# Performance work log

Measured on AMD Instinct MI355X. Metric: run time of the kernel, lower is better.

## Reference

```python
import jax, jax.numpy as jnp
import numpy as np
from jax import lax


def ternarize(w):
    # TWN-style ternarization: threshold delta = 0.7*mean|w|, scale alpha =
    # mean |w| over surviving entries; straight-through in backward.
    aw = jnp.abs(w)
    delta = 0.7 * jnp.mean(aw)
    mask = (aw > delta).astype(w.dtype)
    alpha = jnp.sum(aw * mask) / jnp.maximum(jnp.sum(mask), 1.0)
    q = alpha * jnp.sign(w) * mask
    return w + lax.stop_gradient(q - w)


def conv2d(x, w, b):
    # x: [N,C,H,W], w: [O,I,kh,kw]
    y = lax.conv_general_dilated(x, w, window_strides=(1, 1), padding='VALID',
                                 dimension_numbers=('NCHW', 'OIHW', 'NCHW'))
    return y + b[None, :, None, None]


def maxpool2(x):
    return lax.reduce_window(x, -jnp.inf, lax.max,
                             window_dimensions=(1, 1, 2, 2),
                             window_strides=(1, 1, 2, 2), padding='VALID')


def setup_inputs() -> dict:
    key = jax.random.key(0)
    ks = jax.random.split(key, 11)
    n_classes = 10
    x = jax.random.normal(ks[0], (1024, 1, 32, 32), dtype=jnp.float32)
    # Kaiming-ish scaled params
    w1 = jax.random.normal(ks[1], (32, 1, 5, 5), jnp.float32) * (1.0 / np.sqrt(1 * 25))
    b1 = jnp.zeros((32,), jnp.float32)
    w2 = jax.random.normal(ks[2], (64, 32, 5, 5), jnp.float32) * (1.0 / np.sqrt(32 * 25))
    b2 = jnp.zeros((64,), jnp.float32)
    w3 = jax.random.normal(ks[3], (120, 64, 5, 5), jnp.float32) * (1.0 / np.sqrt(64 * 25))
    b3 = jnp.zeros((120,), jnp.float32)
    fw1 = jax.random.normal(ks[4], (84, 120), jnp.float32) * (1.0 / np.sqrt(120))
    fb1 = jnp.zeros((84,), jnp.float32)
    fw2 = jax.random.normal(ks[5], (n_classes, 84), jnp.float32) * (1.0 / np.sqrt(84))
    fb2 = jnp.zeros((n_classes,), jnp.float32)
    return {"x": x, "w1": w1, "b1": b1, "w2": w2, "b2": b2,
            "w3": w3, "b3": b3, "fw1": fw1, "fb1": fb1, "fw2": fw2, "fb2": fb2}


def reference(x, w1, b1, w2, b2, w3, b3, fw1, fb1, fw2, fb2):
    h = jnp.tanh(conv2d(x, ternarize(w1), b1))   # [N,32,28,28]
    h = maxpool2(h)                              # [N,32,14,14]
    h = jnp.tanh(conv2d(h, ternarize(w2), b2))   # [N,64,10,10]
    h = maxpool2(h)                              # [N,64,5,5]
    h = jnp.tanh(conv2d(h, ternarize(w3), b3))   # [N,120,1,1]
    h = h.reshape(h.shape[0], -1)                # [N,120]
    h = jnp.tanh(h @ ternarize(fw1).T + fb1)     # [N,84]
    logits = h @ ternarize(fw2).T + fb2          # [N,n_classes]
    probs = jax.nn.softmax(logits, axis=1)
    return (logits, probs)
```

## Files before the change

### kernel.cpp

```cpp
#include <hip/hip_runtime.h>
#include <hip/hip_bf16.h>
#include <math.h>


typedef __attribute__((ext_vector_type(8))) short bf16x8;
typedef __attribute__((ext_vector_type(4))) float f32x4;

static const size_t OFF_PB    = 0;
static const size_t OFF_W1B   = 256;
static const size_t OFF_W2B   = 1056;
static const size_t OFF_W3B   = 26656;
static const size_t OFF_FW1T  = 129056;
static const size_t OFF_FW2T  = 139136;
static const size_t OFF_P2B   = 139976;

#define BPT 16

__device__ __forceinline__ ushort f2bf(float v) {
    unsigned u = __float_as_uint(v);
    unsigned r = (u + 0x7FFFu + ((u >> 16) & 1u)) >> 16;
    return (ushort)r;
}
__device__ __forceinline__ float bf2f(ushort h) {
    return __uint_as_float((unsigned)h << 16);
}

__device__ __forceinline__ float tanh_fast(float x) {
    float e = __expf(-2.0f * fabsf(x));
    float r = 1.0f - 2.0f * e / (1.0f + e);
    return copysignf(r, x);
}

__device__ __forceinline__ void tensor_select(int tensor,
        const float* w1, const float* w2, const float* w3,
        const float* fw1, const float* fw2,
        const float*& src, int& O, int& K) {
    switch (tensor) {
        case 0: src = w1;  O = 32;  K = 25;   break;
        case 1: src = w2;  O = 64;  K = 800;  break;
        case 2: src = w3;  O = 120; K = 1600; break;
        case 3: src = fw1; O = 84;  K = 120;  break;
        default: src = fw2; O = 10; K = 84;   break;
    }
}

__device__ __forceinline__ float block_sum_256(float v, float* sbuf) {
    #pragma unroll
    for (int off = 32; off > 0; off >>= 1) v += __shfl_down(v, off);
    const int wid = threadIdx.x >> 6;
    if ((threadIdx.x & 63) == 0) sbuf[wid] = v;
    __syncthreads();
    return sbuf[0] + sbuf[1] + sbuf[2] + sbuf[3];
}

__device__ __forceinline__ float alpha_of(const float* pb, int tensor) {
    float s1 = 0.f, c = 0.f;
    #pragma unroll
    for (int i = 0; i < BPT; ++i) {
        s1 += pb[80 + tensor * BPT + i];
        c  += pb[160 + tensor * BPT + i];
    }
    return s1 / fmaxf(c, 1.0f);
}

__global__ __launch_bounds__(256)
void tern_pass1(const float* w1, const float* w2, const float* w3,
                const float* fw1, const float* fw2, float* pb) {
    __shared__ float sbuf[4];
    const int tensor = blockIdx.x / BPT;
    const int blk    = blockIdx.x % BPT;
    const float* src; int O, K;
    tensor_select(tensor, w1, w2, w3, fw1, fw2, src, O, K);
    const int n = O * K;
    float s = 0.f;
    for (int i = blk * 256 + threadIdx.x; i < n; i += BPT * 256)
        s += fabsf(src[i]);
    s = block_sum_256(s, sbuf);
    if (threadIdx.x == 0) pb[tensor * BPT + blk] = s;
}

__global__ __launch_bounds__(256)
void tern_pass2(const float* w1, const float* w2, const float* w3,
                const float* fw1, const float* fw2,
                ushort* w1b, ushort* w2b, ushort* w3b,
                float* fw1t, float* fw2t, float* pb) {
    __shared__ float sbuf[4];
    const int tensor = blockIdx.x / BPT;
    const int blk    = blockIdx.x % BPT;
    const float* src; int O, K;
    tensor_select(tensor, w1, w2, w3, fw1, fw2, src, O, K);
    const int n = O * K;
    float tot = 0.f;
    #pragma unroll
    for (int i = 0; i < BPT; ++i) tot += pb[tensor * BPT + i];
    const float delta = 0.7f * tot / (float)n;

    const ushort BP = 0x3F80u, BN = 0xBF80u;
    float s1 = 0.f, cnt = 0.f;

    if (tensor == 0) {
        for (int j = blk * 256 + threadIdx.x; j < 1024; j += BPT * 256) {
            const int oc = j >> 5, kk = j & 31;
            ushort qb = 0;
            if (kk < 25) {
                float w = src[oc * 25 + kk];
                float aw = fabsf(w);
                if (aw > delta) { s1 += aw; cnt += 1.f; qb = (w > 0.f) ? BP : BN; }
            }
            w1b[j] = qb;
        }
    } else if (tensor == 2) {
        for (int i = blk * 256 + threadIdx.x; i < 128 * 1600; i += BPT * 256) {
            ushort qb = 0;
            if (i < n) {
                float w = src[i];
                float aw = fabsf(w);
                if (aw > delta) { s1 += aw; cnt += 1.f; qb = (w > 0.f) ? BP : BN; }
            }
            w3b[i] = qb;
        }
    } else if (tensor == 1) {
        for (int i = blk * 256 + threadIdx.x; i < n; i += BPT * 256) {
            float w = src[i];
            float aw = fabsf(w);
            ushort qb = 0;
            if (aw > delta) { s1 += aw; cnt += 1.f; qb = (w > 0.f) ? BP : BN; }
            int oc = i / 800;
            int r  = i - oc * 800;
            int ic = r / 25;
            int tap = r - ic * 25;
            w2b[oc * 800 + tap * 32 + ic] = qb;
        }
    } else {
        float* dst = (tensor == 3) ? fw1t : fw2t;
        for (int i = blk * 256 + threadIdx.x; i < n; i += BPT * 256) {
            float w = src[i];
            float aw = fabsf(w);
            float q = 0.f;
            if (aw > delta) { s1 += aw; cnt += 1.f; q = (w > 0.f) ? 1.f : -1.f; }
            int o = i / K;
            int k = i - o * K;
            dst[k * O + o] = q;
        }
    }
    s1 = block_sum_256(s1, sbuf);
    __syncthreads();
    cnt = block_sum_256(cnt, sbuf);
    if (threadIdx.x == 0) {
        pb[80 + tensor * BPT + blk]  = s1;
        pb[160 + tensor * BPT + blk] = cnt;
    }
}

#define C2PF 4
__device__ __forceinline__ void conv2_all(
        const ushort* __restrict__ w2b, const ushort* sxt,
        int n0, int mt0, int lane, f32x4 acc[4][2]) {
    const int col = lane & 15, quad = lane >> 4;
    const ushort* abase[4];
    #pragma unroll
    for (int mi = 0; mi < 4; ++mi) {
        int m = (mt0 + mi) * 16 + col;
        m = m < 100 ? m : 99;
        const int oh = m / 10, ow = m - oh * 10;
        abase[mi] = sxt + (oh * 14 + ow) * 40 + quad * 8;
    }
    const ushort* wb0 = w2b + (size_t)(n0 + col) * 800 + quad * 8;
    const ushort* wb1 = wb0 + 16 * 800;
    bf16x8 pb0[C2PF], pb1[C2PF];
    #pragma unroll
    for (int i = 0; i < C2PF; ++i) {
        pb0[i] = *(const bf16x8*)(wb0 + i * 32);
        pb1[i] = *(const bf16x8*)(wb1 + i * 32);
    }
    #pragma unroll
    for (int tap = 0; tap < 25; ++tap) {
        const int slot = tap & (C2PF - 1);
        const bf16x8 b0 = pb0[slot];
        const bf16x8 b1 = pb1[slot];
        if (tap + C2PF < 25) {
            pb0[slot] = *(const bf16x8*)(wb0 + (tap + C2PF) * 32);
            pb1[slot] = *(const bf16x8*)(wb1 + (tap + C2PF) * 32);
        }
        const int kh = tap / 5, kw = tap - kh * 5;
        const int aoff = (kh * 14 + kw) * 40;
        #pragma unroll
        for (int mi = 0; mi < 4; ++mi) {
            bf16x8 af = *(const bf16x8*)(abase[mi] + aoff);
            acc[mi][0] = __builtin_amdgcn_mfma_f32_16x16x32_bf16(af, b0, acc[mi][0], 0, 0, 0);
            acc[mi][1] = __builtin_amdgcn_mfma_f32_16x16x32_bf16(af, b1, acc[mi][1], 0, 0, 0);
        }
    }
}

__global__ __launch_bounds__(256, 4)
void conv12_kernel(const float* __restrict__ x, const ushort* __restrict__ w1b,
                   const float* __restrict__ b1, const ushort* __restrict__ w2b,
                   const float* __restrict__ b2, const float* __restrict__ pb,
                   ushort* __restrict__ p2b) {
    __shared__ __align__(16) char smem[37328];
    ushort* A      = (ushort*)smem;
    float*  hb2    = (float*) smem;
    ushort* sxt    = (ushort*)(smem + 19584);
    ushort* sxb    = (ushort*)(smem + 35264);
    float*  salpha = (float*) (smem + 37312);

    const int n = blockIdx.x;
    const int t = threadIdx.x;
    const int wave = t >> 6, lane = t & 63;
    const int col = lane & 15, quad = lane >> 4;

    bf16x8 B0 = *(const bf16x8*)(w1b + col * 32 + quad * 8);
    bf16x8 B1 = *(const bf16x8*)(w1b + (col + 16) * 32 + quad * 8);
    const float b1a = b1[col];
    const float b1b = b1[col + 16];

    {
        float4 v = ((const float4*)(x + (size_t)n * 1024))[t];
        ushort4 q;
        q.x = f2bf(v.x); q.y = f2bf(v.y); q.z = f2bf(v.z); q.w = f2bf(v.w);
        *(ushort4*)(sxb + t * 4) = q;
        if (t == 0) salpha[0] = alpha_of(pb, 0);
        if (t == 1) salpha[1] = alpha_of(pb, 1);
    }
    __syncthreads();

    const float a1 = salpha[0];
    for (int c = 0; c < 3; ++c) {
        const int tbase = (c == 0) ? 0 : (17 + 16 * (c - 1));
        const int ct    = (c == 0) ? 17 : 16;
        const int pbase = tbase * 16;
        const int rows  = ct * 16;

        for (int r = t; r < rows; r += 256) {
            const int p   = pbase + r;
            const int pb4 = p >> 2, sub = p & 3;
            const int oh = 2 * (pb4 / 14) + (sub >> 1);
            const int ow = 2 * (pb4 % 14) + (sub & 1);
            ushort v[25];
            #pragma unroll
            for (int kh = 0; kh < 5; ++kh) {
                const ushort* rr = sxb + (oh + kh) * 32 + ow;
                v[kh*5+0]=rr[0]; v[kh*5+1]=rr[1]; v[kh*5+2]=rr[2];
                v[kh*5+3]=rr[3]; v[kh*5+4]=rr[4];
            }
            uint2* arow = (uint2*)(A + r * 36);
            #pragma unroll
            for (int j = 0; j < 6; ++j) {
                uint2 w;
                w.x = (unsigned)v[4*j]   | ((unsigned)v[4*j+1] << 16);
                w.y = (unsigned)v[4*j+2] | ((unsigned)v[4*j+3] << 16);
                arow[j] = w;
            }
            uint2 w6; w6.x = (unsigned)v[24]; w6.y = 0u;
            arow[6] = w6;
            uint2 w7; w7.x = 0u; w7.y = 0u;
            arow[7] = w7;
        }
        __syncthreads();

        for (int tl = wave; tl < ct; tl += 4) {
            const ushort* ap = A + (tl * 16 + col) * 36 + quad * 8;
            ushort4 lo = *(const ushort4*)ap;
            ushort4 hi = *(const ushort4*)(ap + 4);
            bf16x8 af;
            af[0]=(short)lo.x; af[1]=(short)lo.y; af[2]=(short)lo.z; af[3]=(short)lo.w;
            af[4]=(short)hi.x; af[5]=(short)hi.y; af[6]=(short)hi.z; af[7]=(short)hi.w;
            f32x4 z = {};
            f32x4 c0 = __builtin_amdgcn_mfma_f32_16x16x32_bf16(af, B0, z, 0, 0, 0);
            f32x4 c1 = __builtin_amdgcn_mfma_f32_16x16x32_bf16(af, B1, z, 0, 0, 0);
            const int pos2 = (pbase >> 2) + tl * 4 + quad;
            const float h01 = bf2f(f2bf(fmaxf(c0[0], c0[1])));
            const float h23 = bf2f(f2bf(fmaxf(c0[2], c0[3])));
            sxt[pos2 * 40 + col] =
                f2bf(tanh_fast(fmaf(a1, fmaxf(h01, h23), b1a)));
            const float g01 = bf2f(f2bf(fmaxf(c1[0], c1[1])));
            const float g23 = bf2f(f2bf(fmaxf(c1[2], c1[3])));
            sxt[pos2 * 40 + col + 16] =
                f2bf(tanh_fast(fmaf(a1, fmaxf(g01, g23), b1b)));
        }
        __syncthreads();
    }

    const int n0  = (wave & 1) * 32;
    const int mt0 = (wave >> 1) * 4;
    f32x4 acc2[4][2] = {};
    conv2_all(w2b, sxt, n0, mt0, lane, acc2);

    {
        #pragma unroll
        for (int mi = 0; mi < 4; ++mi) {
            const int mrow = (mt0 + mi) * 16 + quad * 4;
            if (mrow < 100) {
                #pragma unroll
                for (int np = 0; np < 2; ++np) {
                    const int oc = n0 + np * 16 + col;
                    float2 hm;
                    hm.x = fmaxf(acc2[mi][np][0], acc2[mi][np][1]);
                    hm.y = fmaxf(acc2[mi][np][2], acc2[mi][np][3]);
                    *(float2*)(&hb2[oc * 50 + (mrow >> 1)]) = hm;
                }
            }
        }
    }
    __syncthreads();

    const float a2 = salpha[1];
    for (int idx = t; idx < 1600; idx += 256) {
        const int oc = idx / 25, r = idx - oc * 25;
        const int ph = r / 5, pw = r - ph * 5;
        const float* hb = &hb2[oc * 50 + ph * 10 + pw];
        float m = fmaxf(hb[0], hb[5]);
        p2b[(size_t)n * 1600 + idx] = f2bf(tanh_fast(fmaf(a2, m, b2[oc])));
    }
}

__global__ __launch_bounds__(1024)
void conv3fc_kernel(const ushort* __restrict__ p2b, const ushort* __restrict__ w3b,
                    const float* __restrict__ b3, const float* __restrict__ pb,
                    const float* __restrict__ fw1t, const float* __restrict__ fb1,
                    const float* __restrict__ fw2t, const float* __restrict__ fb2,
                    float* __restrict__ out) {
    __shared__ __align__(16) char redmem[32768];
    __shared__ __align__(16) float h3s[16][120];
    __shared__ __align__(16) float fw1s[120 * 84];
    __shared__ __align__(16) float fw2s[84 * 10];
    __shared__ float salpha[3];
    float (*red)[8][4][64] = (float (*)[8][4][64])redmem;
    float* sh4 = (float*)redmem;
    float* sl  = (float*)(redmem + 16 * 84 * 4);

    const int t = threadIdx.x;
    const int wave = t >> 6, lane = t & 63;
    const int col = lane & 15, quad = lane >> 4;
    const int img0 = blockIdx.x * 16;
    const int kg  = wave & 3;
    const int ntg = wave >> 2;

    for (int i = t; i < 2520; i += 1024)
        ((float4*)fw1s)[i] = ((const float4*)fw1t)[i];
    if (t < 210) ((float4*)fw2s)[t] = ((const float4*)fw2t)[t];
    if (t == 0) salpha[0] = alpha_of(pb, 2);
    if (t == 1) salpha[1] = alpha_of(pb, 3);
    if (t == 2) salpha[2] = alpha_of(pb, 4);

    const int kstart = (kg < 2) ? kg * 13 : 26 + (kg - 2) * 12;
    const int steps  = (kg < 2) ? 13 : 12;
    const ushort* Abase = p2b + (size_t)(img0 + col) * 1600 + kstart * 32 + quad * 8;

    f32x4 acc[2] = {};
    {
        const int nt0 = ntg * 2;
        const ushort* Bb0 = w3b + (size_t)(nt0 * 16 + col) * 1600 + kstart * 32 + quad * 8;
        const ushort* Bb1 = Bb0 + (size_t)16 * 1600;
        for (int s = 0; s < steps; ++s) {
            const bf16x8 af = *(const bf16x8*)(Abase + s * 32);
            const bf16x8 b0 = *(const bf16x8*)(Bb0 + s * 32);
            const bf16x8 b1 = *(const bf16x8*)(Bb1 + s * 32);
            acc[0] = __builtin_amdgcn_mfma_f32_16x16x32_bf16(af, b0, acc[0], 0, 0, 0);
            acc[1] = __builtin_amdgcn_mfma_f32_16x16x32_bf16(af, b1, acc[1], 0, 0, 0);
        }
        #pragma unroll
        for (int j = 0; j < 2; ++j)
            #pragma unroll
            for (int r = 0; r < 4; ++r)
                red[kg][nt0 + j][r][lane] = acc[j][r];
    }
    __syncthreads();

    {
        const float a3 = salpha[0];
        #pragma unroll
        for (int half = 0; half < 2; ++half) {
            const int idx = t + half * 1024;
            const int nt  = idx >> 8;
            const int rem = idx & 255;
            const int vh  = rem >> 6;
            const int l   = rem & 63;
            const int img = ((l >> 4) << 2) + vh;
            const int oc  = (nt << 4) + (l & 15);
            if (oc < 120) {
                float s = red[0][nt][vh][l] + red[1][nt][vh][l]
                        + red[2][nt][vh][l] + red[3][nt][vh][l];
                h3s[img][oc] = tanh_fast(fmaf(a3, s, b3[oc]));
            }
        }
    }
    __syncthreads();

    {
        const float af1 = salpha[1];
        for (int task = t; task < 1344; task += 1024) {
            const int img = task / 84, oc = task - img * 84;
            float a = 0.f;
            #pragma unroll 4
            for (int k = 0; k < 120; ++k)
                a = fmaf(fw1s[k * 84 + oc], h3s[img][k], a);
            sh4[img * 84 + oc] = tanh_fast(fmaf(af1, a, fb1[oc]));
        }
    }
    __syncthreads();

    if (t < 160) {
        const float af2 = salpha[2];
        const int img = t / 10, oc = t - img * 10;
        float a2 = 0.f;
        #pragma unroll 4
        for (int k = 0; k < 84; ++k)
            a2 = fmaf(fw2s[k * 10 + oc], sh4[img * 84 + k], a2);
        const float lg = fmaf(af2, a2, fb2[oc]);
        sl[img * 10 + oc] = lg;
        out[(size_t)(img0 + img) * 10 + oc] = lg;
    }
    __syncthreads();

    if (t < 160) {
        const int img = t / 10, oc = t - img * 10;
        float m = -INFINITY;
        #pragma unroll
        for (int i = 0; i < 10; ++i) m = fmaxf(m, sl[img * 10 + i]);
        float s = 0.f;
        #pragma unroll
        for (int i = 0; i < 10; ++i) s += expf(sl[img * 10 + i] - m);
        out[10240 + (size_t)(img0 + img) * 10 + oc] = expf(sl[img * 10 + oc] - m) / s;
    }
}

extern "C" void kernel_launch(void* const* d_in, const int* in_sizes, int n_in,
                              void* d_out, int out_size, void* d_ws, size_t ws_size,
                              hipStream_t stream) {
    const float* x   = (const float*)d_in[0];
    const float* w1  = (const float*)d_in[1];
    const float* b1  = (const float*)d_in[2];
    const float* w2  = (const float*)d_in[3];
    const float* b2  = (const float*)d_in[4];
    const float* w3  = (const float*)d_in[5];
    const float* b3  = (const float*)d_in[6];
    const float* fw1 = (const float*)d_in[7];
    const float* fb1 = (const float*)d_in[8];
    const float* fw2 = (const float*)d_in[9];
    const float* fb2 = (const float*)d_in[10];

    float* ws = (float*)d_ws;
    float*  pb   = ws + OFF_PB;
    ushort* w1b  = (ushort*)(ws + OFF_W1B);
    ushort* w2b  = (ushort*)(ws + OFF_W2B);
    ushort* w3b  = (ushort*)(ws + OFF_W3B);
    float*  fw1t = ws + OFF_FW1T;
    float*  fw2t = ws + OFF_FW2T;
    ushort* p2b  = (ushort*)(ws + OFF_P2B);
    float*  out  = (float*)d_out;

    tern_pass1<<<5 * BPT, 256, 0, stream>>>(w1, w2, w3, fw1, fw2, pb);
    tern_pass2<<<5 * BPT, 256, 0, stream>>>(w1, w2, w3, fw1, fw2,
                                            w1b, w2b, w3b, fw1t, fw2t, pb);
    conv12_kernel<<<1024, 256, 0, stream>>>(x, w1b, b1, w2b, b2, pb, p2b);
    conv3fc_kernel<<<64, 1024, 0, stream>>>(p2b, w3b, b3, pb,
                                            fw1t, fb1, fw2t, fb2, out);
}
```

Before: 153.0 us.

## Gather conv1 im2col fragments directly into registers, drop LDS staging buffer

Conv1 no longer builds an im2col matrix in shared memory across three chunks with barriers. Each lane now gathers its eight bf16 taps straight from the input image in LDS into an MFMA A-fragment, using precomputed tap offsets and a mask for the padded K range. This removes the staging writes and reads plus four barriers, and shrinks the LDS footprint so more blocks may fit per CU. The cost is eight scattered 16-bit LDS reads per lane per tile, which may cause bank conflicts.

Measured after the change: 148.5 us. 2.9% less time.

```diff
diff --git a/kernel.cpp b/kernel.cpp
--- a/kernel.cpp
+++ b/kernel.cpp
@@ -198,12 +198,11 @@
                    const float* __restrict__ b1, const ushort* __restrict__ w2b,
                    const float* __restrict__ b2, const float* __restrict__ pb,
                    ushort* __restrict__ p2b) {
-    __shared__ __align__(16) char smem[37328];
-    ushort* A      = (ushort*)smem;
-    float*  hb2    = (float*) smem;
-    ushort* sxt    = (ushort*)(smem + 19584);
-    ushort* sxb    = (ushort*)(smem + 35264);
-    float*  salpha = (float*) (smem + 37312);
+    __shared__ __align__(16) char smem[30544];
+    ushort* sxt    = (ushort*)smem;
+    float*  hb2    = (float*) (smem + 15680);
+    ushort* sxb    = (ushort*)(smem + 28480);
+    float*  salpha = (float*) (smem + 30528);
 
     const int n = blockIdx.x;
     const int t = threadIdx.x;
@@ -225,51 +224,42 @@
     }
     __syncthreads();
 
-    const float a1 = salpha[0];
-    for (int c = 0; c < 3; ++c) {
-        const int tbase = (c == 0) ? 0 : (17 + 16 * (c - 1));
-        const int ct    = (c == 0) ? 17 : 16;
-        const int pbase = tbase * 16;
-        const int rows  = ct * 16;
-
-        for (int r = t; r < rows; r += 256) {
-            const int p   = pbase + r;
-            const int pb4 = p >> 2, sub = p & 3;
-            const int oh = 2 * (pb4 / 14) + (sub >> 1);
-            const int ow = 2 * (pb4 % 14) + (sub & 1);
-            ushort v[25];
-            #pragma unroll
-            for (int kh = 0; kh < 5; ++kh) {
-                const ushort* rr = sxb + (oh + kh) * 32 + ow;
-                v[kh*5+0]=rr[0]; v[kh*5+1]=rr[1]; v[kh*5+2]=rr[2];
-                v[kh*5+3]=rr[3]; v[kh*5+4]=rr[4];
-            }
-            uint2* arow = (uint2*)(A + r * 36);
-            #pragma unroll
-            for (int j = 0; j < 6; ++j) {
-                uint2 w;
-                w.x = (unsigned)v[4*j]   | ((unsigned)v[4*j+1] << 16);
-                w.y = (unsigned)v[4*j+2] | ((unsigned)v[4*j+3] << 16);
-                arow[j] = w;
-            }
-            uint2 w6; w6.x = (unsigned)v[24]; w6.y = 0u;
-            arow[6] = w6;
-            uint2 w7; w7.x = 0u; w7.y = 0u;
-            arow[7] = w7;
-        }
-        __syncthreads();
-
-        for (int tl = wave; tl < ct; tl += 4) {
-            const ushort* ap = A + (tl * 16 + col) * 36 + quad * 8;
-            ushort4 lo = *(const ushort4*)ap;
-            ushort4 hi = *(const ushort4*)(ap + 4);
-            bf16x8 af;
-            af[0]=(short)lo.x; af[1]=(short)lo.y; af[2]=(short)lo.z; af[3]=(short)lo.w;
-            af[4]=(short)hi.x; af[5]=(short)hi.y; af[6]=(short)hi.z; af[7]=(short)hi.w;
+    {
+        const float a1 = salpha[0];
+        const int sub  = col & 3;
+        const int colq = col >> 2;
+        const int soff = ((sub >> 1) << 5) + (sub & 1);
+        int woff[8];
+        #pragma unroll
+        for (int j = 0; j < 8; ++j) {
+            const int tap = quad * 8 + j;
+            woff[j] = (tap < 25) ? ((tap / 5) << 5) + (tap % 5) : 0;
+        }
+        const unsigned kmask = (quad == 3) ? 0u : 0xFFFFFFFFu;
+
+        for (int tl = wave; tl < 49; tl += 4) {
+            const int pb4 = tl * 4 + colq;
+            const int bh  = (pb4 * 4682) >> 16;
+            const int bw  = pb4 - bh * 14;
+            const int base = (bh << 6) + (bw << 1) + soff;
+            unsigned v0 = sxb[base + woff[0]];
+            unsigned v1 = sxb[base + woff[1]] & kmask;
+            unsigned v2 = sxb[base + woff[2]] & kmask;
+            unsigned v3 = sxb[base + woff[3]] & kmask;
+            unsigned v4 = sxb[base + woff[4]] & kmask;
+            unsigned v5 = sxb[base + woff[5]] & kmask;
+            unsigned v6 = sxb[base + woff[6]] & kmask;
+            unsigned v7 = sxb[base + woff[7]] & kmask;
+            uint4 u;
+            u.x = v0 | (v1 << 16);
+            u.y = v2 | (v3 << 16);
+            u.z = v4 | (v5 << 16);
+            u.w = v6 | (v7 << 16);
+            const bf16x8 af = *(const bf16x8*)&u;
             f32x4 z = {};
             f32x4 c0 = __builtin_amdgcn_mfma_f32_16x16x32_bf16(af, B0, z, 0, 0, 0);
             f32x4 c1 = __builtin_amdgcn_mfma_f32_16x16x32_bf16(af, B1, z, 0, 0, 0);
-            const int pos2 = (pbase >> 2) + tl * 4 + quad;
+            const int pos2 = tl * 4 + quad;
             const float h01 = bf2f(f2bf(fmaxf(c0[0], c0[1])));
             const float h23 = bf2f(f2bf(fmaxf(c0[2], c0[3])));
             sxt[pos2 * 40 + col] =
@@ -279,8 +269,8 @@
             sxt[pos2 * 40 + col + 16] =
                 f2bf(tanh_fast(fmaf(a1, fmaxf(g01, g23), b1b)));
         }
-        __syncthreads();
-    }
+    }
+    __syncthreads();
 
     const int n0  = (wave & 1) * 32;
     const int mt0 = (wave >> 1) * 4;
```
